# Kernel tuning notes

Hardware: AMD Instinct MI355X
Metric: run time of the kernel (lower is better)

## Reference

```python
import jax, jax.numpy as jnp
import numpy as np

N = 100000
E = 1600000
D_IN = 128
D_H = 128


def setup_inputs() -> dict:
    key = jax.random.key(0)
    ks = jax.random.split(key, 8)
    x = jax.random.normal(ks[0], (N, D_IN), dtype=jnp.float32)
    edge_index = jax.random.randint(ks[1], (2, E), 0, N, dtype=jnp.int64)
    # Glorot-ish init for weights, zeros for biases (PyG GCNConv default: glorot W, zero bias)
    W1 = jax.random.normal(ks[2], (D_IN, D_H), dtype=jnp.float32) / np.sqrt(D_IN)
    b1 = jnp.zeros((D_H,), dtype=jnp.float32)
    W2 = jax.random.normal(ks[3], (D_H, D_H), dtype=jnp.float32) / np.sqrt(D_H)
    b2 = jnp.zeros((D_H,), dtype=jnp.float32)
    Wout = jax.random.normal(ks[4], (D_H, 1), dtype=jnp.float32) / np.sqrt(D_H)
    bout = jnp.zeros((1,), dtype=jnp.float32)
    return {"x": x, "edge_index": edge_index, "W1": W1, "b1": b1,
            "W2": W2, "b2": b2, "Wout": Wout, "bout": bout}


def _gcn_conv(x, W, b, src, dst, inv_sqrt_deg, inv_deg):
    # PyG GCNConv: h = x @ W; out = sum_{j in N(i)} norm_ij * h_j + (1/deg_i) * h_i + b
    # norm_ij = deg_i^-1/2 * deg_j^-1/2 with self-loops folded into deg.
    h = x @ W                                   # [N, D]
    norm = inv_sqrt_deg[src] * inv_sqrt_deg[dst]  # [E]
    msgs = h[src] * norm[:, None]               # [E, D] gather
    agg = jax.ops.segment_sum(msgs, dst, num_segments=x.shape[0])  # [N, D] scatter
    agg = agg + h * inv_deg[:, None]            # self-loop term (norm = 1/deg)
    return agg + b


def reference(x, edge_index, W1, b1, W2, b2, Wout, bout):
    src = edge_index[0]
    dst = edge_index[1]
    n = x.shape[0]
    # degree with self-loops: deg_i = 1 + #incoming edges to i
    deg = 1.0 + jax.ops.segment_sum(jnp.ones((src.shape[0],), dtype=x.dtype), dst, num_segments=n)
    inv_sqrt_deg = jax.lax.rsqrt(deg)
    inv_deg = 1.0 / deg
    h = jax.nn.relu(_gcn_conv(x, W1, b1, src, dst, inv_sqrt_deg, inv_deg))
    h = jax.nn.relu(_gcn_conv(h, W2, b2, src, dst, inv_sqrt_deg, inv_deg))
    logits = h @ Wout + bout                    # [N, 1]
    return jax.nn.sigmoid(logits).squeeze(-1)   # [N]
```

## Files before the change

kernel.cpp:

```cpp
#include <hip/hip_runtime.h>
#include <cstddef>

#define CAPD 64
#define BSZ 512
#define BSH 9
#define CHUNK 8192
#define BCAP 12288

typedef unsigned int uint;
typedef unsigned short ushort;
typedef unsigned char uchar;
typedef float f32x4 __attribute__((ext_vector_type(4)));
typedef _Float16 f16x8 __attribute__((ext_vector_type(8)));

__device__ inline float h_lo(uint v) {
    union { ushort u; _Float16 h; } c; c.u = (ushort)(v & 0xFFFFu); return (float)c.h;
}
__device__ inline float h_hi(uint v) {
    union { ushort u; _Float16 h; } c; c.u = (ushort)(v >> 16); return (float)c.h;
}
__device__ inline ushort h_bits(float x) {
    union { _Float16 h; ushort u; } c; c.h = (_Float16)x; return c.u;
}
__device__ inline uint h_pack(float a, float b) {
    return (uint)h_bits(a) | ((uint)h_bits(b) << 16);
}
__device__ inline float i8f(uint v, int k) {
    return (float)((int)(v << ((3 - k) * 8)) >> 24);
}

__global__ __launch_bounds__(256) void p3_scatter(const int* __restrict__ esrc,
                                                  const int* __restrict__ edst, int E,
                                                  int nb,
                                                  int* __restrict__ bucketCursor,
                                                  unsigned* __restrict__ gSorted) {
    __shared__ unsigned payL[CHUNK];
    __shared__ uchar    bktL[CHUNK];
    __shared__ unsigned outL[CHUNK];
    __shared__ int hist[256], segoff[256], cursor[256], gbase[256], sc[256];
    int bid = blockIdx.x, tid = threadIdx.x;
    int e0 = bid * CHUNK;
    int m = min(E - e0, CHUNK);
    for (int i = tid; i < m; i += 256) {
        unsigned d = (unsigned)edst[e0 + i];
        unsigned s = (unsigned)esrc[e0 + i];
        payL[i] = s | ((d & (BSZ - 1)) << 23);
        bktL[i] = (uchar)(d >> BSH);
    }
    hist[tid] = 0;
    __syncthreads();
    for (int i = tid; i < m; i += 256)
        atomicAdd(&hist[bktL[i]], 1);
    __syncthreads();
    sc[tid] = hist[tid];
    __syncthreads();
    for (int off = 1; off < 256; off <<= 1) {
        int v = (tid >= off) ? sc[tid - off] : 0;
        __syncthreads();
        sc[tid] += v;
        __syncthreads();
    }
    segoff[tid] = sc[tid] - hist[tid];
    cursor[tid] = segoff[tid];
    if (tid < nb && hist[tid] > 0) gbase[tid] = atomicAdd(&bucketCursor[tid], hist[tid]);
    __syncthreads();
    for (int i = tid; i < m; i += 256) {
        int b = (int)bktL[i];
        int p = atomicAdd(&cursor[b], 1);
        outL[p] = payL[i];
    }
    __syncthreads();
    int wave = tid >> 6, lane = tid & 63;
    for (int b = wave; b < nb; b += 4) {
        int off = segoff[b], len = hist[b];
        if (len == 0) continue;
        int gb = gbase[b];
        unsigned* dst = gSorted + (size_t)b * BCAP;
        for (int i = lane; i < len; i += 64)
            if (gb + i < BCAP) dst[gb + i] = outL[off + i];
    }
}

__global__ __launch_bounds__(256) void p4_build(const unsigned* __restrict__ gSorted,
                                                const int* __restrict__ bucketCursor,
                                                int nb, int N, int* __restrict__ cnt,
                                                float* __restrict__ isd,
                                                int* __restrict__ ell,
                                                const float* __restrict__ W1,
                                                const float* __restrict__ W2,
                                                uint* __restrict__ Wt1,
                                                uint* __restrict__ Wt2) {
    __shared__ unsigned ellL[BSZ * CAPD];
    __shared__ int cntL[BSZ];
    int b = blockIdx.x, tid = threadIdx.x;
    if (b >= nb) {
        const float* W = (b - nb) ? W2 : W1;
        uint* O = (b - nb) ? Wt2 : Wt1;
        float (*ws)[129] = (float(*)[129])ellL;
#pragma unroll
        for (int j = 0; j < 16; ++j) {
            int q = tid + 256 * j;
            int k = q >> 5, c = (q & 31) * 4;
            float4 v = *reinterpret_cast<const float4*>(W + k * 128 + c);
            ws[k][c] = v.x; ws[k][c + 1] = v.y; ws[k][c + 2] = v.z; ws[k][c + 3] = v.w;
        }
        __syncthreads();
#pragma unroll
        for (int j = 0; j < 32; ++j) {
            int q = tid + 256 * j;
            int ncol = q >> 6, kw = q & 63;
            O[q] = h_pack(ws[2 * kw][ncol], ws[2 * kw + 1][ncol]);
        }
        return;
    }
    int n0 = b * BSZ;
    for (int i = tid; i < BSZ; i += 256) cntL[i] = 0;
    __syncthreads();
    int len = bucketCursor[b];
    if (len > BCAP) len = BCAP;
    const unsigned* seg = gSorted + (size_t)b * BCAP;
    for (int i = tid; i < len; i += 256) {
        unsigned e = seg[i];
        int dl = (int)(e >> 23);
        int src = (int)(e & 0x7FFFFFu);
        int p = atomicAdd(&cntL[dl], 1);
        if (p < CAPD) ellL[dl * CAPD + p] = (unsigned)src;
    }
    __syncthreads();
    int nValid = min(BSZ, N - n0);
    int total = nValid * CAPD;
    const int* ellLi = (const int*)ellL;
    for (int i = tid; i < total; i += 256) {
        int row = i >> 6, pos = i & 63;
        int c = cntL[row];
        if (pos < min(c, CAPD))
            ell[(size_t)n0 * CAPD + i] = ellLi[i];
    }
    for (int i = tid; i < nValid; i += 256) {
        int c = cntL[i];
        cnt[n0 + i] = c;
        isd[n0 + i] = rsqrtf(1.0f + (float)c);
    }
}

__global__ __launch_bounds__(256) void gemm_mfma(const void* __restrict__ A, int aF16,
                                                 const uint* __restrict__ Wt,
                                                 const float* __restrict__ scale,
                                                 uint* __restrict__ Tq,
                                                 float* __restrict__ Ts, int n) {
    __shared__ uint SH[16384];
    char* shb = (char*)SH;
    const int tid = threadIdx.x;
    const int m0 = blockIdx.x * 128;

    if (aF16) {
        const uint* Af = (const uint*)A;
#pragma unroll
        for (int j = 0; j < 8; ++j) {
            int q = tid + 256 * j;
            int row = q >> 4, c16 = q & 15;
            int grow = m0 + row;
            uint4 v = make_uint4(0u, 0u, 0u, 0u);
            if (grow < n) v = *reinterpret_cast<const uint4*>(Af + (size_t)grow * 64 + c16 * 4);
            *reinterpret_cast<uint4*>(shb + row * 256 + ((c16 * 16) ^ ((row & 7) << 4))) = v;
        }
    } else {
        const float* Af = (const float*)A;
#pragma unroll
        for (int j = 0; j < 8; ++j) {
            int q = tid + 256 * j;
            int row = q >> 4, c16 = q & 15;
            int grow = m0 + row;
            uint4 o = make_uint4(0u, 0u, 0u, 0u);
            if (grow < n) {
                float4 v0 = *reinterpret_cast<const float4*>(Af + (size_t)grow * 128 + c16 * 8);
                float4 v1 = *reinterpret_cast<const float4*>(Af + (size_t)grow * 128 + c16 * 8 + 4);
                o.x = h_pack(v0.x, v0.y); o.y = h_pack(v0.z, v0.w);
                o.z = h_pack(v1.x, v1.y); o.w = h_pack(v1.z, v1.w);
            }
            *reinterpret_cast<uint4*>(shb + row * 256 + ((c16 * 16) ^ ((row & 7) << 4))) = o;
        }
    }
#pragma unroll
    for (int j = 0; j < 8; ++j) {
        int q = tid + 256 * j;
        int col = q >> 4, c16 = q & 15;
        uint4 v = *reinterpret_cast<const uint4*>(Wt + col * 64 + c16 * 4);
        *reinterpret_cast<uint4*>(shb + 32768 + col * 256 + ((c16 * 16) ^ ((col & 7) << 4))) = v;
    }
    __syncthreads();

    const int w = tid >> 6, l = tid & 63;
    const int lrow = l & 15, kg = l >> 4;
    const int swz = (lrow & 7) << 4;

    f32x4 acc[2][8] = {};
#pragma unroll
    for (int kk = 0; kk < 4; ++kk) {
        const int koff = (kk * 64 + kg * 16) ^ swz;
        f16x8 a[2], b[8];
#pragma unroll
        for (int mr = 0; mr < 2; ++mr) {
            int r = w * 32 + mr * 16 + lrow;
            a[mr] = *reinterpret_cast<const f16x8*>(shb + r * 256 + koff);
        }
#pragma unroll
        for (int nc = 0; nc < 8; ++nc) {
            int c = nc * 16 + lrow;
            b[nc] = *reinterpret_cast<const f16x8*>(shb + 32768 + c * 256 + koff);
        }
#pragma unroll
        for (int mr = 0; mr < 2; ++mr)
#pragma unroll
            for (int nc = 0; nc < 8; ++nc)
                acc[mr][nc] = __builtin_amdgcn_mfma_f32_16x16x32_f16(a[mr], b[nc], acc[mr][nc], 0, 0, 0);
    }
    __syncthreads();

    ushort* Cs = (ushort*)SH;
#pragma unroll
    for (int mr = 0; mr < 2; ++mr) {
        int rb = w * 32 + mr * 16 + kg * 4;
#pragma unroll
        for (int i = 0; i < 4; ++i) {
            int grow = m0 + rb + i;
            float s = (grow < n) ? scale[grow] : 0.f;
#pragma unroll
            for (int nc = 0; nc < 8; ++nc)
                Cs[(rb + i) * 136 + nc * 16 + lrow] = h_bits(s * acc[mr][nc][i]);
        }
    }
    __syncthreads();
    const uint* Cw = (const uint*)SH;
#pragma unroll
    for (int j = 0; j < 8; ++j) {
        int q = tid + 256 * j;
        int row = q >> 4, c8 = q & 15;
        int grow = m0 + row;
        uint4 v = *reinterpret_cast<const uint4*>(Cw + row * 68 + c8 * 4);
        float f0 = h_lo(v.x), f1 = h_hi(v.x), f2 = h_lo(v.y), f3 = h_hi(v.y);
        float f4 = h_lo(v.z), f5 = h_hi(v.z), f6 = h_lo(v.w), f7 = h_hi(v.w);
        float mx = fmaxf(fmaxf(fmaxf(fabsf(f0), fabsf(f1)), fmaxf(fabsf(f2), fabsf(f3))),
                         fmaxf(fmaxf(fabsf(f4), fabsf(f5)), fmaxf(fabsf(f6), fabsf(f7))));
#pragma unroll
        for (int off = 8; off > 0; off >>= 1) mx = fmaxf(mx, __shfl_xor(mx, off, 16));
        mx = fmaxf(mx, 1e-20f);
        float inv = 127.f / mx;
        int q0 = (int)rintf(f0 * inv), q1 = (int)rintf(f1 * inv);
        int q2 = (int)rintf(f2 * inv), q3 = (int)rintf(f3 * inv);
        int q4 = (int)rintf(f4 * inv), q5 = (int)rintf(f5 * inv);
        int q6 = (int)rintf(f6 * inv), q7 = (int)rintf(f7 * inv);
        uint w0 = (uint)(q0 & 0xFF) | ((uint)(q1 & 0xFF) << 8) |
                  ((uint)(q2 & 0xFF) << 16) | ((uint)(q3 & 0xFF) << 24);
        uint w1 = (uint)(q4 & 0xFF) | ((uint)(q5 & 0xFF) << 8) |
                  ((uint)(q6 & 0xFF) << 16) | ((uint)(q7 & 0xFF) << 24);
        if (grow < n) {
            *reinterpret_cast<uint2*>(Tq + (size_t)grow * 32 + c8 * 2) = make_uint2(w0, w1);
            if (c8 == 0) Ts[grow] = mx * (1.f / 127.f);
        }
    }
}

__global__ __launch_bounds__(256) void agg_kernel(const uint* __restrict__ Tq,
                                                  const float* __restrict__ Ts,
                                                  const int* __restrict__ ell,
                                                  const int* __restrict__ cnt,
                                                  const float* __restrict__ isd,
                                                  const float* __restrict__ bias,
                                                  uint* __restrict__ Hb, int n) {
    int node = (int)((blockIdx.x * 256 + threadIdx.x) >> 5);
    int ln = threadIdx.x & 31;
    if (node >= n) return;
    float di = isd[node];
    int c = cnt[node];
    if (c > CAPD) c = CAPD;
    const int* row = ell + (size_t)node * CAPD;
    float a0, a1, a2, a3;
    {
        uint v = Tq[(size_t)node * 32 + ln];
        float sc = Ts[node];
        a0 = sc * i8f(v, 0); a1 = sc * i8f(v, 1); a2 = sc * i8f(v, 2); a3 = sc * i8f(v, 3);
    }
    int j = 0;
    for (; j + 8 <= c; j += 8) {
        int4 sa = *reinterpret_cast<const int4*>(row + j);
        int4 sb = *reinterpret_cast<const int4*>(row + j + 4);
        uint v0 = Tq[(size_t)sa.x * 32 + ln]; float c0 = Ts[sa.x];
        uint v1 = Tq[(size_t)sa.y * 32 + ln]; float c1 = Ts[sa.y];
        uint v2 = Tq[(size_t)sa.z * 32 + ln]; float c2 = Ts[sa.z];
        uint v3 = Tq[(size_t)sa.w * 32 + ln]; float c3 = Ts[sa.w];
        uint v4 = Tq[(size_t)sb.x * 32 + ln]; float c4 = Ts[sb.x];
        uint v5 = Tq[(size_t)sb.y * 32 + ln]; float c5 = Ts[sb.y];
        uint v6 = Tq[(size_t)sb.z * 32 + ln]; float c6 = Ts[sb.z];
        uint v7 = Tq[(size_t)sb.w * 32 + ln]; float c7 = Ts[sb.w];
#pragma unroll
        for (int k = 0; k < 4; ++k) {
            float t = fmaf(c0, i8f(v0, k), fmaf(c1, i8f(v1, k),
                      fmaf(c2, i8f(v2, k), fmaf(c3, i8f(v3, k),
                      fmaf(c4, i8f(v4, k), fmaf(c5, i8f(v5, k),
                      fmaf(c6, i8f(v6, k), c7 * i8f(v7, k))))))));
            if (k == 0) a0 += t; else if (k == 1) a1 += t; else if (k == 2) a2 += t; else a3 += t;
        }
    }
    for (; j + 4 <= c; j += 4) {
        int4 s4 = *reinterpret_cast<const int4*>(row + j);
        uint v0 = Tq[(size_t)s4.x * 32 + ln]; float c0 = Ts[s4.x];
        uint v1 = Tq[(size_t)s4.y * 32 + ln]; float c1 = Ts[s4.y];
        uint v2 = Tq[(size_t)s4.z * 32 + ln]; float c2 = Ts[s4.z];
        uint v3 = Tq[(size_t)s4.w * 32 + ln]; float c3 = Ts[s4.w];
        a0 += fmaf(c0, i8f(v0, 0), fmaf(c1, i8f(v1, 0), fmaf(c2, i8f(v2, 0), c3 * i8f(v3, 0))));
        a1 += fmaf(c0, i8f(v0, 1), fmaf(c1, i8f(v1, 1), fmaf(c2, i8f(v2, 1), c3 * i8f(v3, 1))));
        a2 += fmaf(c0, i8f(v0, 2), fmaf(c1, i8f(v1, 2), fmaf(c2, i8f(v2, 2), c3 * i8f(v3, 2))));
        a3 += fmaf(c0, i8f(v0, 3), fmaf(c1, i8f(v1, 3), fmaf(c2, i8f(v2, 3), c3 * i8f(v3, 3))));
    }
    for (; j < c; ++j) {
        int s = row[j];
        uint v = Tq[(size_t)s * 32 + ln];
        float sc = Ts[s];
        a0 = fmaf(sc, i8f(v, 0), a0); a1 = fmaf(sc, i8f(v, 1), a1);
        a2 = fmaf(sc, i8f(v, 2), a2); a3 = fmaf(sc, i8f(v, 3), a3);
    }
    float4 bv = *reinterpret_cast<const float4*>(bias + ln * 4);
    float h0 = fmaxf(fmaf(di, a0, bv.x), 0.f);
    float h1 = fmaxf(fmaf(di, a1, bv.y), 0.f);
    float h2 = fmaxf(fmaf(di, a2, bv.z), 0.f);
    float h3 = fmaxf(fmaf(di, a3, bv.w), 0.f);
    *reinterpret_cast<uint2*>(Hb + (size_t)node * 64 + ln * 2) =
        make_uint2(h_pack(h0, h1), h_pack(h2, h3));
}

__global__ __launch_bounds__(256) void agg_out_kernel(const uint* __restrict__ Tq,
                                                      const float* __restrict__ Ts,
                                                      const int* __restrict__ ell,
                                                      const int* __restrict__ cnt,
                                                      const float* __restrict__ isd,
                                                      const float* __restrict__ bias,
                                                      const float* __restrict__ Wout,
                                                      const float* __restrict__ bout,
                                                      float* __restrict__ out, int n) {
    int node = (int)((blockIdx.x * 256 + threadIdx.x) >> 5);
    int ln = threadIdx.x & 31;
    if (node >= n) return;
    float di = isd[node];
    int c = cnt[node];
    if (c > CAPD) c = CAPD;
    const int* row = ell + (size_t)node * CAPD;
    float a0, a1, a2, a3;
    {
        uint v = Tq[(size_t)node * 32 + ln];
        float sc = Ts[node];
        a0 = sc * i8f(v, 0); a1 = sc * i8f(v, 1); a2 = sc * i8f(v, 2); a3 = sc * i8f(v, 3);
    }
    int j = 0;
    for (; j + 8 <= c; j += 8) {
        int4 sa = *reinterpret_cast<const int4*>(row + j);
        int4 sb = *reinterpret_cast<const int4*>(row + j + 4);
        uint v0 = Tq[(size_t)sa.x * 32 + ln]; float c0 = Ts[sa.x];
        uint v1 = Tq[(size_t)sa.y * 32 + ln]; float c1 = Ts[sa.y];
        uint v2 = Tq[(size_t)sa.z * 32 + ln]; float c2 = Ts[sa.z];
        uint v3 = Tq[(size_t)sa.w * 32 + ln]; float c3 = Ts[sa.w];
        uint v4 = Tq[(size_t)sb.x * 32 + ln]; float c4 = Ts[sb.x];
        uint v5 = Tq[(size_t)sb.y * 32 + ln]; float c5 = Ts[sb.y];
        uint v6 = Tq[(size_t)sb.z * 32 + ln]; float c6 = Ts[sb.z];
        uint v7 = Tq[(size_t)sb.w * 32 + ln]; float c7 = Ts[sb.w];
#pragma unroll
        for (int k = 0; k < 4; ++k) {
            float t = fmaf(c0, i8f(v0, k), fmaf(c1, i8f(v1, k),
                      fmaf(c2, i8f(v2, k), fmaf(c3, i8f(v3, k),
                      fmaf(c4, i8f(v4, k), fmaf(c5, i8f(v5, k),
                      fmaf(c6, i8f(v6, k), c7 * i8f(v7, k))))))));
            if (k == 0) a0 += t; else if (k == 1) a1 += t; else if (k == 2) a2 += t; else a3 += t;
        }
    }
    for (; j + 4 <= c; j += 4) {
        int4 s4 = *reinterpret_cast<const int4*>(row + j);
        uint v0 = Tq[(size_t)s4.x * 32 + ln]; float c0 = Ts[s4.x];
        uint v1 = Tq[(size_t)s4.y * 32 + ln]; float c1 = Ts[s4.y];
        uint v2 = Tq[(size_t)s4.z * 32 + ln]; float c2 = Ts[s4.z];
        uint v3 = Tq[(size_t)s4.w * 32 + ln]; float c3 = Ts[s4.w];
        a0 += fmaf(c0, i8f(v0, 0), fmaf(c1, i8f(v1, 0), fmaf(c2, i8f(v2, 0), c3 * i8f(v3, 0))));
        a1 += fmaf(c0, i8f(v0, 1), fmaf(c1, i8f(v1, 1), fmaf(c2, i8f(v2, 1), c3 * i8f(v3, 1))));
        a2 += fmaf(c0, i8f(v0, 2), fmaf(c1, i8f(v1, 2), fmaf(c2, i8f(v2, 2), c3 * i8f(v3, 2))));
        a3 += fmaf(c0, i8f(v0, 3), fmaf(c1, i8f(v1, 3), fmaf(c2, i8f(v2, 3), c3 * i8f(v3, 3))));
    }
    for (; j < c; ++j) {
        int s = row[j];
        uint v = Tq[(size_t)s * 32 + ln];
        float sc = Ts[s];
        a0 = fmaf(sc, i8f(v, 0), a0); a1 = fmaf(sc, i8f(v, 1), a1);
        a2 = fmaf(sc, i8f(v, 2), a2); a3 = fmaf(sc, i8f(v, 3), a3);
    }
    float4 bv = *reinterpret_cast<const float4*>(bias + ln * 4);
    float4 wv = *reinterpret_cast<const float4*>(Wout + ln * 4);
    float h0 = fmaxf(fmaf(di, a0, bv.x), 0.f);
    float h1 = fmaxf(fmaf(di, a1, bv.y), 0.f);
    float h2 = fmaxf(fmaf(di, a2, bv.z), 0.f);
    float h3 = fmaxf(fmaf(di, a3, bv.w), 0.f);
    float v = fmaf(h0, wv.x, fmaf(h1, wv.y, fmaf(h2, wv.z, h3 * wv.w)));
#pragma unroll
    for (int off = 16; off > 0; off >>= 1) v += __shfl_xor(v, off, 32);
    if (ln == 0) out[node] = 1.f / (1.f + expf(-(v + bout[0])));
}

extern "C" void kernel_launch(void* const* d_in, const int* in_sizes, int n_in,
                              void* d_out, int out_size, void* d_ws, size_t ws_size,
                              hipStream_t stream) {
    const float* x    = (const float*)d_in[0];
    const int*   ei   = (const int*)d_in[1];
    const float* W1   = (const float*)d_in[2];
    const float* b1   = (const float*)d_in[3];
    const float* W2   = (const float*)d_in[4];
    const float* b2   = (const float*)d_in[5];
    const float* Wout = (const float*)d_in[6];
    const float* bout = (const float*)d_in[7];
    float* out = (float*)d_out;

    const int N = in_sizes[0] / 128;
    const int E = in_sizes[1] / 2;
    const int* esrc = ei;
    const int* edst = ei + E;

    char* p = (char*)d_ws;
    auto alloc = [&](size_t bytes) {
        char* r = p;
        p += (bytes + 255) & ~(size_t)255;
        return (void*)r;
    };
    int*   cnt = (int*)  alloc((size_t)N * 4);
    float* isd = (float*)alloc((size_t)N * 4);
    int*   ell = (int*)  alloc((size_t)N * CAPD * 4);
    uint*  Tq  = (uint*) alloc((size_t)N * 32 * 4);
    float* Ts  = (float*)alloc((size_t)N * 4);
    uint*  Hb  = (uint*) alloc((size_t)N * 64 * 4);
    uint*  Wt1 = (uint*) alloc(8192 * 4);
    uint*  Wt2 = (uint*) alloc(8192 * 4);

    const int nb  = (N + BSZ - 1) / BSZ;
    const int NB2 = (E + CHUNK - 1) / CHUNK;
    char* q = (char*)Tq;
    auto alloc2 = [&](size_t bytes) {
        char* r = q;
        q += (bytes + 255) & ~(size_t)255;
        return (void*)r;
    };
    unsigned* gSorted      = (unsigned*)alloc2((size_t)nb * BCAP * 4);
    int*      bucketCursor = (int*)     alloc2((size_t)nb * 4);

    hipMemsetAsync(bucketCursor, 0, (size_t)nb * 4, stream);
    p3_scatter<<<NB2,    256, 0, stream>>>(esrc, edst, E, nb, bucketCursor, gSorted);
    p4_build  <<<nb + 2, 256, 0, stream>>>(gSorted, bucketCursor, nb, N, cnt, isd, ell,
                                           W1, W2, Wt1, Wt2);

    const int gblocks = (N + 127) / 128;
    const int ablocks = (N + 7) / 8;
    gemm_mfma<<<gblocks, 256, 0, stream>>>(x, 0, Wt1, isd, Tq, Ts, N);
    agg_kernel<<<ablocks, 256, 0, stream>>>(Tq, Ts, ell, cnt, isd, b1, Hb, N);
    gemm_mfma<<<gblocks, 256, 0, stream>>>(Hb, 1, Wt2, isd, Tq, Ts, N);
    agg_out_kernel<<<ablocks, 256, 0, stream>>>(Tq, Ts, ell, cnt, isd, b2, Wout, bout, out, N);
}
```

Before: 189.2 us.

## Fuse ELL build with first GEMM and move degree scaling into aggregation

Moves the weight transpose into the scatter kernel and merges the ELL build (now split into half-buckets of 256 rows) with the first-layer GEMM in one launch, so the two run concurrently. Because the layer-1 GEMM no longer depends on degrees, the source-side inverse-sqrt-degree factor is applied inside aggregation through an extra isd gather per edge. Quantization moves from signed int8 to offset-128 unsigned bytes with a running scale-sum correction, which makes the byte-to-float conversion cheaper. gSorted gets its own workspace region instead of aliasing Tq, so the fused kernel can write Tq safely, at the cost of more workspace and extra gather traffic in agg_kernel.

```diff
diff --git a/kernel.cpp b/kernel.cpp
--- a/kernel.cpp
+++ b/kernel.cpp
@@ -25,20 +25,50 @@
 __device__ inline uint h_pack(float a, float b) {
     return (uint)h_bits(a) | ((uint)h_bits(b) << 16);
 }
-__device__ inline float i8f(uint v, int k) {
-    return (float)((int)(v << ((3 - k) * 8)) >> 24);
-}
+__device__ inline float ub0(uint v) { return (float)(v & 0xFFu); }
+__device__ inline float ub1(uint v) { return (float)((v >> 8) & 0xFFu); }
+__device__ inline float ub2(uint v) { return (float)((v >> 16) & 0xFFu); }
+__device__ inline float ub3(uint v) { return (float)(v >> 24); }
 
 __global__ __launch_bounds__(256) void p3_scatter(const int* __restrict__ esrc,
                                                   const int* __restrict__ edst, int E,
-                                                  int nb,
+                                                  int nb, int NB2,
                                                   int* __restrict__ bucketCursor,
-                                                  unsigned* __restrict__ gSorted) {
-    __shared__ unsigned payL[CHUNK];
-    __shared__ uchar    bktL[CHUNK];
-    __shared__ unsigned outL[CHUNK];
-    __shared__ int hist[256], segoff[256], cursor[256], gbase[256], sc[256];
+                                                  unsigned* __restrict__ gSorted,
+                                                  const float* __restrict__ W1,
+                                                  const float* __restrict__ W2,
+                                                  uint* __restrict__ Wt1,
+                                                  uint* __restrict__ Wt2) {
+    __shared__ __align__(16) char SHB[78848];
     int bid = blockIdx.x, tid = threadIdx.x;
+    if (bid >= NB2) {
+        const float* W = (bid - NB2) ? W2 : W1;
+        uint* O = (bid - NB2) ? Wt2 : Wt1;
+        float (*ws)[129] = (float(*)[129])SHB;
+#pragma unroll
+        for (int j = 0; j < 16; ++j) {
+            int q = tid + 256 * j;
+            int k = q >> 5, c = (q & 31) * 4;
+            float4 v = *reinterpret_cast<const float4*>(W + k * 128 + c);
+            ws[k][c] = v.x; ws[k][c + 1] = v.y; ws[k][c + 2] = v.z; ws[k][c + 3] = v.w;
+        }
+        __syncthreads();
+#pragma unroll
+        for (int j = 0; j < 32; ++j) {
+            int q = tid + 256 * j;
+            int ncol = q >> 6, kw = q & 63;
+            O[q] = h_pack(ws[2 * kw][ncol], ws[2 * kw + 1][ncol]);
+        }
+        return;
+    }
+    uint*  payL = (uint*)SHB;
+    uint*  outL = (uint*)(SHB + 32768);
+    uchar* bktL = (uchar*)(SHB + 65536);
+    int*   hist   = (int*)(SHB + 73728);
+    int*   segoff = hist + 256;
+    int*   cursor = segoff + 256;
+    int*   gbase  = cursor + 256;
+    int*   sc     = gbase + 256;
     int e0 = bid * CHUNK;
     int m = min(E - e0, CHUNK);
     for (int i = tid; i < m; i += 256) {
@@ -81,78 +111,13 @@
     }
 }
 
-__global__ __launch_bounds__(256) void p4_build(const unsigned* __restrict__ gSorted,
-                                                const int* __restrict__ bucketCursor,
-                                                int nb, int N, int* __restrict__ cnt,
-                                                float* __restrict__ isd,
-                                                int* __restrict__ ell,
-                                                const float* __restrict__ W1,
-                                                const float* __restrict__ W2,
-                                                uint* __restrict__ Wt1,
-                                                uint* __restrict__ Wt2) {
-    __shared__ unsigned ellL[BSZ * CAPD];
-    __shared__ int cntL[BSZ];
-    int b = blockIdx.x, tid = threadIdx.x;
-    if (b >= nb) {
-        const float* W = (b - nb) ? W2 : W1;
-        uint* O = (b - nb) ? Wt2 : Wt1;
-        float (*ws)[129] = (float(*)[129])ellL;
-#pragma unroll
-        for (int j = 0; j < 16; ++j) {
-            int q = tid + 256 * j;
-            int k = q >> 5, c = (q & 31) * 4;
-            float4 v = *reinterpret_cast<const float4*>(W + k * 128 + c);
-            ws[k][c] = v.x; ws[k][c + 1] = v.y; ws[k][c + 2] = v.z; ws[k][c + 3] = v.w;
-        }
-        __syncthreads();
-#pragma unroll
-        for (int j = 0; j < 32; ++j) {
-            int q = tid + 256 * j;
-            int ncol = q >> 6, kw = q & 63;
-            O[q] = h_pack(ws[2 * kw][ncol], ws[2 * kw + 1][ncol]);
-        }
-        return;
-    }
-    int n0 = b * BSZ;
-    for (int i = tid; i < BSZ; i += 256) cntL[i] = 0;
-    __syncthreads();
-    int len = bucketCursor[b];
-    if (len > BCAP) len = BCAP;
-    const unsigned* seg = gSorted + (size_t)b * BCAP;
-    for (int i = tid; i < len; i += 256) {
-        unsigned e = seg[i];
-        int dl = (int)(e >> 23);
-        int src = (int)(e & 0x7FFFFFu);
-        int p = atomicAdd(&cntL[dl], 1);
-        if (p < CAPD) ellL[dl * CAPD + p] = (unsigned)src;
-    }
-    __syncthreads();
-    int nValid = min(BSZ, N - n0);
-    int total = nValid * CAPD;
-    const int* ellLi = (const int*)ellL;
-    for (int i = tid; i < total; i += 256) {
-        int row = i >> 6, pos = i & 63;
-        int c = cntL[row];
-        if (pos < min(c, CAPD))
-            ell[(size_t)n0 * CAPD + i] = ellLi[i];
-    }
-    for (int i = tid; i < nValid; i += 256) {
-        int c = cntL[i];
-        cnt[n0 + i] = c;
-        isd[n0 + i] = rsqrtf(1.0f + (float)c);
-    }
-}
-
-__global__ __launch_bounds__(256) void gemm_mfma(const void* __restrict__ A, int aF16,
-                                                 const uint* __restrict__ Wt,
-                                                 const float* __restrict__ scale,
-                                                 uint* __restrict__ Tq,
-                                                 float* __restrict__ Ts, int n) {
-    __shared__ uint SH[16384];
+__device__ __forceinline__ void gemm_core(const void* __restrict__ A, int aF16,
+                                          const uint* __restrict__ Wt,
+                                          const float* __restrict__ scale,
+                                          uint* __restrict__ Tq,
+                                          float* __restrict__ Ts,
+                                          int n, int m0, int tid, uint* SH) {
     char* shb = (char*)SH;
-    const int tid = threadIdx.x;
-    const int m0 = blockIdx.x * 128;
-
     if (aF16) {
         const uint* Af = (const uint*)A;
 #pragma unroll
@@ -224,7 +189,7 @@
 #pragma unroll
         for (int i = 0; i < 4; ++i) {
             int grow = m0 + rb + i;
-            float s = (grow < n) ? scale[grow] : 0.f;
+            float s = scale ? ((grow < n) ? scale[grow] : 0.f) : 1.f;
 #pragma unroll
             for (int nc = 0; nc < 8; ++nc)
                 Cs[(rb + i) * 136 + nc * 16 + lrow] = h_bits(s * acc[mr][nc][i]);
@@ -246,19 +211,80 @@
         for (int off = 8; off > 0; off >>= 1) mx = fmaxf(mx, __shfl_xor(mx, off, 16));
         mx = fmaxf(mx, 1e-20f);
         float inv = 127.f / mx;
-        int q0 = (int)rintf(f0 * inv), q1 = (int)rintf(f1 * inv);
-        int q2 = (int)rintf(f2 * inv), q3 = (int)rintf(f3 * inv);
-        int q4 = (int)rintf(f4 * inv), q5 = (int)rintf(f5 * inv);
-        int q6 = (int)rintf(f6 * inv), q7 = (int)rintf(f7 * inv);
-        uint w0 = (uint)(q0 & 0xFF) | ((uint)(q1 & 0xFF) << 8) |
-                  ((uint)(q2 & 0xFF) << 16) | ((uint)(q3 & 0xFF) << 24);
-        uint w1 = (uint)(q4 & 0xFF) | ((uint)(q5 & 0xFF) << 8) |
-                  ((uint)(q6 & 0xFF) << 16) | ((uint)(q7 & 0xFF) << 24);
+        int q0 = (int)rintf(f0 * inv) + 128, q1 = (int)rintf(f1 * inv) + 128;
+        int q2 = (int)rintf(f2 * inv) + 128, q3 = (int)rintf(f3 * inv) + 128;
+        int q4 = (int)rintf(f4 * inv) + 128, q5 = (int)rintf(f5 * inv) + 128;
+        int q6 = (int)rintf(f6 * inv) + 128, q7 = (int)rintf(f7 * inv) + 128;
+        uint w0 = (uint)q0 | ((uint)q1 << 8) | ((uint)q2 << 16) | ((uint)q3 << 24);
+        uint w1 = (uint)q4 | ((uint)q5 << 8) | ((uint)q6 << 16) | ((uint)q7 << 24);
         if (grow < n) {
             *reinterpret_cast<uint2*>(Tq + (size_t)grow * 32 + c8 * 2) = make_uint2(w0, w1);
             if (c8 == 0) Ts[grow] = mx * (1.f / 127.f);
         }
     }
+}
+
+__global__ __launch_bounds__(256) void p4_mega(const unsigned* __restrict__ gSorted,
+                                               const int* __restrict__ bucketCursor,
+                                               int nb, int N,
+                                               int* __restrict__ cnt,
+                                               float* __restrict__ isd,
+                                               int* __restrict__ ell,
+                                               const float* __restrict__ x,
+                                               const uint* __restrict__ Wt1,
+                                               uint* __restrict__ Tq,
+                                               float* __restrict__ Ts) {
+    __shared__ __align__(16) uint SH[16384];
+    __shared__ int cntL[256];
+    int bid = blockIdx.x, tid = threadIdx.x;
+    if (bid < 2 * nb) {
+        int bucket = bid >> 1;
+        unsigned half = (unsigned)(bid & 1);
+        int n0 = bid * 256;
+        uint* ellL = SH;
+        cntL[tid] = 0;
+        __syncthreads();
+        int len = bucketCursor[bucket];
+        if (len > BCAP) len = BCAP;
+        const unsigned* seg = gSorted + (size_t)bucket * BCAP;
+        for (int i = tid; i < len; i += 256) {
+            unsigned e = seg[i];
+            unsigned dl = e >> 23;
+            if ((dl >> 8) == half) {
+                int r = (int)(dl & 255u);
+                int p = atomicAdd(&cntL[r], 1);
+                if (p < CAPD) ellL[r * CAPD + p] = e & 0x7FFFFFu;
+            }
+        }
+        __syncthreads();
+        int nValid = min(256, N - n0);
+        if (nValid > 0) {
+            int total = nValid * CAPD;
+            const int* ellLi = (const int*)ellL;
+            for (int i = tid; i < total; i += 256) {
+                int row = i >> 6, pos = i & 63;
+                int c = cntL[row];
+                if (pos < min(c, CAPD))
+                    ell[(size_t)n0 * CAPD + i] = ellLi[i];
+            }
+            for (int i = tid; i < nValid; i += 256) {
+                int c = cntL[i];
+                cnt[n0 + i] = c;
+                isd[n0 + i] = rsqrtf(1.0f + (float)c);
+            }
+        }
+    } else {
+        gemm_core(x, 0, Wt1, nullptr, Tq, Ts, N, (bid - 2 * nb) * 128, tid, SH);
+    }
+}
+
+__global__ __launch_bounds__(256) void gemm2_kernel(const uint* __restrict__ Hb,
+                                                    const uint* __restrict__ Wt,
+                                                    const float* __restrict__ isd,
+                                                    uint* __restrict__ Tq,
+                                                    float* __restrict__ Ts, int n) {
+    __shared__ __align__(16) uint SH[16384];
+    gemm_core(Hb, 1, Wt, isd, Tq, Ts, n, blockIdx.x * 128, threadIdx.x, SH);
 }
 
 __global__ __launch_bounds__(256) void agg_kernel(const uint* __restrict__ Tq,
@@ -275,56 +301,61 @@
     int c = cnt[node];
     if (c > CAPD) c = CAPD;
     const int* row = ell + (size_t)node * CAPD;
-    float a0, a1, a2, a3;
+    float a0, a1, a2, a3, ssum;
     {
         uint v = Tq[(size_t)node * 32 + ln];
-        float sc = Ts[node];
-        a0 = sc * i8f(v, 0); a1 = sc * i8f(v, 1); a2 = sc * i8f(v, 2); a3 = sc * i8f(v, 3);
+        float sc = Ts[node] * di;
+        ssum = sc;
+        a0 = sc * ub0(v); a1 = sc * ub1(v); a2 = sc * ub2(v); a3 = sc * ub3(v);
     }
     int j = 0;
     for (; j + 8 <= c; j += 8) {
         int4 sa = *reinterpret_cast<const int4*>(row + j);
         int4 sb = *reinterpret_cast<const int4*>(row + j + 4);
-        uint v0 = Tq[(size_t)sa.x * 32 + ln]; float c0 = Ts[sa.x];
-        uint v1 = Tq[(size_t)sa.y * 32 + ln]; float c1 = Ts[sa.y];
-        uint v2 = Tq[(size_t)sa.z * 32 + ln]; float c2 = Ts[sa.z];
-        uint v3 = Tq[(size_t)sa.w * 32 + ln]; float c3 = Ts[sa.w];
-        uint v4 = Tq[(size_t)sb.x * 32 + ln]; float c4 = Ts[sb.x];
-        uint v5 = Tq[(size_t)sb.y * 32 + ln]; float c5 = Ts[sb.y];
-        uint v6 = Tq[(size_t)sb.z * 32 + ln]; float c6 = Ts[sb.z];
-        uint v7 = Tq[(size_t)sb.w * 32 + ln]; float c7 = Ts[sb.w];
-#pragma unroll
-        for (int k = 0; k < 4; ++k) {
-            float t = fmaf(c0, i8f(v0, k), fmaf(c1, i8f(v1, k),
-                      fmaf(c2, i8f(v2, k), fmaf(c3, i8f(v3, k),
-                      fmaf(c4, i8f(v4, k), fmaf(c5, i8f(v5, k),
-                      fmaf(c6, i8f(v6, k), c7 * i8f(v7, k))))))));
-            if (k == 0) a0 += t; else if (k == 1) a1 += t; else if (k == 2) a2 += t; else a3 += t;
-        }
+        uint v0 = Tq[(size_t)sa.x * 32 + ln]; float c0 = Ts[sa.x] * isd[sa.x];
+        uint v1 = Tq[(size_t)sa.y * 32 + ln]; float c1 = Ts[sa.y] * isd[sa.y];
+        uint v2 = Tq[(size_t)sa.z * 32 + ln]; float c2 = Ts[sa.z] * isd[sa.z];
+        uint v3 = Tq[(size_t)sa.w * 32 + ln]; float c3 = Ts[sa.w] * isd[sa.w];
+        uint v4 = Tq[(size_t)sb.x * 32 + ln]; float c4 = Ts[sb.x] * isd[sb.x];
+        uint v5 = Tq[(size_t)sb.y * 32 + ln]; float c5 = Ts[sb.y] * isd[sb.y];
+        uint v6 = Tq[(size_t)sb.z * 32 + ln]; float c6 = Ts[sb.z] * isd[sb.z];
+        uint v7 = Tq[(size_t)sb.w * 32 + ln]; float c7 = Ts[sb.w] * isd[sb.w];
+        ssum += ((c0 + c1) + (c2 + c3)) + ((c4 + c5) + (c6 + c7));
+        a0 = fmaf(c0, ub0(v0), fmaf(c1, ub0(v1), fmaf(c2, ub0(v2), fmaf(c3, ub0(v3),
+             fmaf(c4, ub0(v4), fmaf(c5, ub0(v5), fmaf(c6, ub0(v6), fmaf(c7, ub0(v7), a0))))))));
+        a1 = fmaf(c0, ub1(v0), fmaf(c1, ub1(v1), fmaf(c2, ub1(v2), fmaf(c3, ub1(v3),
+             fmaf(c4, ub1(v4), fmaf(c5, ub1(v5), fmaf(c6, ub1(v6), fmaf(c7, ub1(v7), a1))))))));
+        a2 = fmaf(c0, ub2(v0), fmaf(c1, ub2(v1), fmaf(c2, ub2(v2), fmaf(c3, ub2(v3),
+             fmaf(c4, ub2(v4), fmaf(c5, ub2(v5), fmaf(c6, ub2(v6), fmaf(c7, ub2(v7), a2))))))));
+        a3 = fmaf(c0, ub3(v0), fmaf(c1, ub3(v1), fmaf(c2, ub3(v2), fmaf(c3, ub3(v3),
+             fmaf(c4, ub3(v4), fmaf(c5, ub3(v5), fmaf(c6, ub3(v6), fmaf(c7, ub3(v7), a3))))))));
     }
     for (; j + 4 <= c; j += 4) {
         int4 s4 = *reinterpret_cast<const int4*>(row + j);
-        uint v0 = Tq[(size_t)s4.x * 32 + ln]; float c0 = Ts[s4.x];
-        uint v1 = Tq[(size_t)s4.y * 32 + ln]; float c1 = Ts[s4.y];
-        uint v2 = Tq[(size_t)s4.z * 32 + ln]; float c2 = Ts[s4.z];
-        uint v3 = Tq[(size_t)s4.w * 32 + ln]; float c3 = Ts[s4.w];
-        a0 += fmaf(c0, i8f(v0, 0), fmaf(c1, i8f(v1, 0), fmaf(c2, i8f(v2, 0), c3 * i8f(v3, 0))));
-        a1 += fmaf(c0, i8f(v0, 1), fmaf(c1, i8f(v1, 1), fmaf(c2, i8f(v2, 1), c3 * i8f(v3, 1))));
-        a2 += fmaf(c0, i8f(v0, 2), fmaf(c1, i8f(v1, 2), fmaf(c2, i8f(v2, 2), c3 * i8f(v3, 2))));
-        a3 += fmaf(c0, i8f(v0, 3), fmaf(c1, i8f(v1, 3), fmaf(c2, i8f(v2, 3), c3 * i8f(v3, 3))));
+        uint v0 = Tq[(size_t)s4.x * 32 + ln]; float c0 = Ts[s4.x] * isd[s4.x];
+        uint v1 = Tq[(size_t)s4.y * 32 + ln]; float c1 = Ts[s4.y] * isd[s4.y];
+        uint v2 = Tq[(size_t)s4.z * 32 + ln]; float c2 = Ts[s4.z] * isd[s4.z];
+        uint v3 = Tq[(size_t)s4.w * 32 + ln]; float c3 = Ts[s4.w] * isd[s4.w];
+        ssum += (c0 + c1) + (c2 + c3);
+        a0 = fmaf(c0, ub0(v0), fmaf(c1, ub0(v1), fmaf(c2, ub0(v2), fmaf(c3, ub0(v3), a0))));
+        a1 = fmaf(c0, ub1(v0), fmaf(c1, ub1(v1), fmaf(c2, ub1(v2), fmaf(c3, ub1(v3), a1))));
+        a2 = fmaf(c0, ub2(v0), fmaf(c1, ub2(v1), fmaf(c2, ub2(v2), fmaf(c3, ub2(v3), a2))));
+        a3 = fmaf(c0, ub3(v0), fmaf(c1, ub3(v1), fmaf(c2, ub3(v2), fmaf(c3, ub3(v3), a3))));
     }
     for (; j < c; ++j) {
         int s = row[j];
         uint v = Tq[(size_t)s * 32 + ln];
-        float sc = Ts[s];
-        a0 = fmaf(sc, i8f(v, 0), a0); a1 = fmaf(sc, i8f(v, 1), a1);
-        a2 = fmaf(sc, i8f(v, 2), a2); a3 = fmaf(sc, i8f(v, 3), a3);
-    }
+        float sc = Ts[s] * isd[s];
+        ssum += sc;
+        a0 = fmaf(sc, ub0(v), a0); a1 = fmaf(sc, ub1(v), a1);
+        a2 = fmaf(sc, ub2(v), a2); a3 = fmaf(sc, ub3(v), a3);
+    }
+    float off = 128.f * ssum;
     float4 bv = *reinterpret_cast<const float4*>(bias + ln * 4);
-    float h0 = fmaxf(fmaf(di, a0, bv.x), 0.f);
-    float h1 = fmaxf(fmaf(di, a1, bv.y), 0.f);
-    float h2 = fmaxf(fmaf(di, a2, bv.z), 0.f);
-    float h3 = fmaxf(fmaf(di, a3, bv.w), 0.f);
+    float h0 = fmaxf(fmaf(di, a0 - off, bv.x), 0.f);
+    float h1 = fmaxf(fmaf(di, a1 - off, bv.y), 0.f);
+    float h2 = fmaxf(fmaf(di, a2 - off, bv.z), 0.f);
+    float h3 = fmaxf(fmaf(di, a3 - off, bv.w), 0.f);
     *reinterpret_cast<uint2*>(Hb + (size_t)node * 64 + ln * 2) =
         make_uint2(h_pack(h0, h1), h_pack(h2, h3));
 }
@@ -345,11 +376,12 @@
     int c = cnt[node];
     if (c > CAPD) c = CAPD;
     const int* row = ell + (size_t)node * CAPD;
-    float a0, a1, a2, a3;
+    float a0, a1, a2, a3, ssum;
     {
         uint v = Tq[(size_t)node * 32 + ln];
         float sc = Ts[node];
-        a0 = sc * i8f(v, 0); a1 = sc * i8f(v, 1); a2 = sc * i8f(v, 2); a3 = sc * i8f(v, 3);
+        ssum = sc;
+        a0 = sc * ub0(v); a1 = sc * ub1(v); a2 = sc * ub2(v); a3 = sc * ub3(v);
     }
     int j = 0;
     for (; j + 8 <= c; j += 8) {
@@ -363,14 +395,15 @@
         uint v5 = Tq[(size_t)sb.y * 32 + ln]; float c5 = Ts[sb.y];
         uint v6 = Tq[(size_t)sb.z * 32 + ln]; float c6 = Ts[sb.z];
         uint v7 = Tq[(size_t)sb.w * 32 + ln]; float c7 = Ts[sb.w];
-#pragma unroll
-        for (int k = 0; k < 4; ++k) {
-            float t = fmaf(c0, i8f(v0, k), fmaf(c1, i8f(v1, k),
-                      fmaf(c2, i8f(v2, k), fmaf(c3, i8f(v3, k),
-                      fmaf(c4, i8f(v4, k), fmaf(c5, i8f(v5, k),
-                      fmaf(c6, i8f(v6, k), c7 * i8f(v7, k))))))));
-            if (k == 0) a0 += t; else if (k == 1) a1 += t; else if (k == 2) a2 += t; else a3 += t;
-        }
+        ssum += ((c0 + c1) + (c2 + c3)) + ((c4 + c5) + (c6 + c7));
+        a0 = fmaf(c0, ub0(v0), fmaf(c1, ub0(v1), fmaf(c2, ub0(v2), fmaf(c3, ub0(v3),
+             fmaf(c4, ub0(v4), fmaf(c5, ub0(v5), fmaf(c6, ub0(v6), fmaf(c7, ub0(v7), a0))))))));
+        a1 = fmaf(c0, ub1(v0), fmaf(c1, ub1(v1), fmaf(c2, ub1(v2), fmaf(c3, ub1(v3),
+             fmaf(c4, ub1(v4), fmaf(c5, ub1(v5), fmaf(c6, ub1(v6), fmaf(c7, ub1(v7), a1))))))));
+        a2 = fmaf(c0, ub2(v0), fmaf(c1, ub2(v1), fmaf(c2, ub2(v2), fmaf(c3, ub2(v3),
+             fmaf(c4, ub2(v4), fmaf(c5, ub2(v5), fmaf(c6, ub2(v6), fmaf(c7, ub2(v7), a2))))))));
+        a3 = fmaf(c0, ub3(v0), fmaf(c1, ub3(v1), fmaf(c2, ub3(v2), fmaf(c3, ub3(v3),
+             fmaf(c4, ub3(v4), fmaf(c5, ub3(v5), fmaf(c6, ub3(v6), fmaf(c7, ub3(v7), a3))))))));
     }
     for (; j + 4 <= c; j += 4) {
         int4 s4 = *reinterpret_cast<const int4*>(row + j);
@@ -378,27 +411,30 @@
         uint v1 = Tq[(size_t)s4.y * 32 + ln]; float c1 = Ts[s4.y];
         uint v2 = Tq[(size_t)s4.z * 32 + ln]; float c2 = Ts[s4.z];
         uint v3 = Tq[(size_t)s4.w * 32 + ln]; float c3 = Ts[s4.w];
-        a0 += fmaf(c0, i8f(v0, 0), fmaf(c1, i8f(v1, 0), fmaf(c2, i8f(v2, 0), c3 * i8f(v3, 0))));
-        a1 += fmaf(c0, i8f(v0, 1), fmaf(c1, i8f(v1, 1), fmaf(c2, i8f(v2, 1), c3 * i8f(v3, 1))));
-        a2 += fmaf(c0, i8f(v0, 2), fmaf(c1, i8f(v1, 2), fmaf(c2, i8f(v2, 2), c3 * i8f(v3, 2))));
-        a3 += fmaf(c0, i8f(v0, 3), fmaf(c1, i8f(v1, 3), fmaf(c2, i8f(v2, 3), c3 * i8f(v3, 3))));
+        ssum += (c0 + c1) + (c2 + c3);
+        a0 = fmaf(c0, ub0(v0), fmaf(c1, ub0(v1), fmaf(c2, ub0(v2), fmaf(c3, ub0(v3), a0))));
+        a1 = fmaf(c0, ub1(v0), fmaf(c1, ub1(v1), fmaf(c2, ub1(v2), fmaf(c3, ub1(v3), a1))));
+        a2 = fmaf(c0, ub2(v0), fmaf(c1, ub2(v1), fmaf(c2, ub2(v2), fmaf(c3, ub2(v3), a2))));
+        a3 = fmaf(c0, ub3(v0), fmaf(c1, ub3(v1), fmaf(c2, ub3(v2), fmaf(c3, ub3(v3), a3))));
     }
     for (; j < c; ++j) {
         int s = row[j];
         uint v = Tq[(size_t)s * 32 + ln];
         float sc = Ts[s];
-        a0 = fmaf(sc, i8f(v, 0), a0); a1 = fmaf(sc, i8f(v, 1), a1);
-        a2 = fmaf(sc, i8f(v, 2), a2); a3 = fmaf(sc, i8f(v, 3), a3);
-    }
+        ssum += sc;
+        a0 = fmaf(sc, ub0(v), a0); a1 = fmaf(sc, ub1(v), a1);
+        a2 = fmaf(sc, ub2(v), a2); a3 = fmaf(sc, ub3(v), a3);
+    }
+    float off = 128.f * ssum;
     float4 bv = *reinterpret_cast<const float4*>(bias + ln * 4);
     float4 wv = *reinterpret_cast<const float4*>(Wout + ln * 4);
-    float h0 = fmaxf(fmaf(di, a0, bv.x), 0.f);
-    float h1 = fmaxf(fmaf(di, a1, bv.y), 0.f);
-    float h2 = fmaxf(fmaf(di, a2, bv.z), 0.f);
-    float h3 = fmaxf(fmaf(di, a3, bv.w), 0.f);
+    float h0 = fmaxf(fmaf(di, a0 - off, bv.x), 0.f);
+    float h1 = fmaxf(fmaf(di, a1 - off, bv.y), 0.f);
+    float h2 = fmaxf(fmaf(di, a2 - off, bv.z), 0.f);
+    float h3 = fmaxf(fmaf(di, a3 - off, bv.w), 0.f);
     float v = fmaf(h0, wv.x, fmaf(h1, wv.y, fmaf(h2, wv.z, h3 * wv.w)));
 #pragma unroll
-    for (int off = 16; off > 0; off >>= 1) v += __shfl_xor(v, off, 32);
+    for (int off2 = 16; off2 > 0; off2 >>= 1) v += __shfl_xor(v, off2, 32);
     if (ln == 0) out[node] = 1.f / (1.f + expf(-(v + bout[0])));
 }
 
@@ -426,6 +462,9 @@
         p += (bytes + 255) & ~(size_t)255;
         return (void*)r;
     };
+    const int nb  = (N + BSZ - 1) / BSZ;
+    const int NB2 = (E + CHUNK - 1) / CHUNK;
+
     int*   cnt = (int*)  alloc((size_t)N * 4);
     float* isd = (float*)alloc((size_t)N * 4);
     int*   ell = (int*)  alloc((size_t)N * CAPD * 4);
@@ -434,27 +473,18 @@
     uint*  Hb  = (uint*) alloc((size_t)N * 64 * 4);
     uint*  Wt1 = (uint*) alloc(8192 * 4);
     uint*  Wt2 = (uint*) alloc(8192 * 4);
-
-    const int nb  = (N + BSZ - 1) / BSZ;
-    const int NB2 = (E + CHUNK - 1) / CHUNK;
-    char* q = (char*)Tq;
-    auto alloc2 = [&](size_t bytes) {
-        char* r = q;
-        q += (bytes + 255) & ~(size_t)255;
-        return (void*)r;
-    };
-    unsigned* gSorted      = (unsigned*)alloc2((size_t)nb * BCAP * 4);
-    int*      bucketCursor = (int*)     alloc2((size_t)nb * 4);
+    unsigned* gSorted      = (unsigned*)alloc((size_t)nb * BCAP * 4);
+    int*      bucketCursor = (int*)     alloc((size_t)nb * 4);
 
     hipMemsetAsync(bucketCursor, 0, (size_t)nb * 4, stream);
-    p3_scatter<<<NB2,    256, 0, stream>>>(esrc, edst, E, nb, bucketCursor, gSorted);
-    p4_build  <<<nb + 2, 256, 0, stream>>>(gSorted, bucketCursor, nb, N, cnt, isd, ell,
-                                           W1, W2, Wt1, Wt2);
+    p3_scatter<<<NB2 + 2, 256, 0, stream>>>(esrc, edst, E, nb, NB2, bucketCursor, gSorted,
+                                            W1, W2, Wt1, Wt2);
 
     const int gblocks = (N + 127) / 128;
     const int ablocks = (N + 7) / 8;
-    gemm_mfma<<<gblocks, 256, 0, stream>>>(x, 0, Wt1, isd, Tq, Ts, N);
+    p4_mega<<<2 * nb + gblocks, 256, 0, stream>>>(gSorted, bucketCursor, nb, N,
+                                                  cnt, isd, ell, x, Wt1, Tq, Ts);
     agg_kernel<<<ablocks, 256, 0, stream>>>(Tq, Ts, ell, cnt, isd, b1, Hb, N);
-    gemm_mfma<<<gblocks, 256, 0, stream>>>(Hb, 1, Wt2, isd, Tq, Ts, N);
+    gemm2_kernel<<<gblocks, 256, 0, stream>>>(Hb, Wt2, isd, Tq, Ts, N);
     agg_out_kernel<<<ablocks, 256, 0, stream>>>(Tq, Ts, ell, cnt, isd, b2, Wout, bout, out, N);
 }
```

Result: no change. 188.1 us (-0.6%).
